# Performance work log

Measured on AMD Instinct MI355X. Metric: run time of the kernel, lower is better.

## Reference

```python
import jax, jax.numpy as jnp
import numpy as np
from jax import lax

D = 1024      # embedding_dim
E = 8         # num_experts
F = 4096      # expert_dim
TOP_K = 2


def setup_inputs() -> dict:
    key = jax.random.key(0)
    ks = jax.random.split(key, 8)
    s = 0.02
    return {
        "x": jax.random.normal(ks[0], (4, 2048, D), dtype=jnp.float32),
        "gate_w": jax.random.normal(ks[1], (D, E), dtype=jnp.float32) * s,
        "gate_b": jnp.zeros((E,), dtype=jnp.float32),
        "w1": jax.random.normal(ks[2], (E, D, F), dtype=jnp.float32) * s,
        "b1": jnp.zeros((E, F), dtype=jnp.float32),
        "w2": jax.random.normal(ks[3], (E, F, D), dtype=jnp.float32) * s,
        "b2": jnp.zeros((E, D), dtype=jnp.float32),
    }


def reference(x, gate_w, gate_b, w1, b1, w2, b2):
    B, S, _ = x.shape
    flat = x.reshape(-1, D)                      # [T, D]
    T = flat.shape[0]

    # Router: top-k gating with softmax over the selected logits (in fp32)
    logits = flat @ gate_w + gate_b              # [T, E]
    topv, topi = lax.top_k(logits, TOP_K)        # [T, K]
    topw = jax.nn.softmax(topv.astype(jnp.float32), axis=-1).astype(x.dtype)
    routing = jnp.zeros_like(logits).at[jnp.arange(T)[:, None], topi].set(topw)  # [T, E]

    # Per-expert MLP, combined with routing weights (zeros for unselected experts
    # reproduce the masked gather/scatter of the original exactly).
    def body(acc, params):
        W1e, b1e, W2e, b2e, we = params          # we: [T]
        h = jax.nn.gelu(flat @ W1e + b1e, approximate=False)  # [T, F]
        out = h @ W2e + b2e                      # [T, D]
        return acc + out * we[:, None], None

    init = jnp.zeros_like(flat)
    final, _ = lax.scan(body, init, (w1, b1, w2, b2, routing.T))
    return final.reshape(B, S, D)
```

## Files before the change

### kernel.cpp

```cpp
#include <hip/hip_runtime.h>
#include <hip/hip_bf16.h>
#include <math.h>


#define TK 8192
#define DDIM 1024
#define FDIM 4096
#define NEXP 8
#define MAXT128 136

typedef unsigned short u16;
typedef __attribute__((ext_vector_type(8))) short bf16x8;
typedef __attribute__((ext_vector_type(4))) float f32x4;

typedef const __attribute__((address_space(1))) unsigned int* gp_u32;
typedef __attribute__((address_space(3))) unsigned int* lp_u32;

__device__ __forceinline__ u16 f2bf(float f) {
  unsigned x = __float_as_uint(f);
  x += 0x7fffu + ((x >> 16) & 1u);
  return (u16)(x >> 16);
}

__device__ __forceinline__ float fast_gelu(float v) {
  float p = v * (1.5957691216f + 0.0713548162f * v * v);
  float t = __expf(p);
  return v * t * __builtin_amdgcn_rcpf(t + 1.0f);
}

__device__ __forceinline__ bf16x8 ldfrag(const char* base, int row, int slot) {
  return *(const bf16x8*)(base + row * 128 + ((slot ^ (row & 7)) << 4));
}

__global__ void router_kernel(const float* __restrict__ x, const float* __restrict__ gw,
                              const float* __restrict__ gb,
                              int* __restrict__ top_e, float* __restrict__ top_w) {
  const int t = blockIdx.x;
  const int l = threadIdx.x;
  const float* xr = x + (size_t)t * DDIM;
  float acc[8] = {0, 0, 0, 0, 0, 0, 0, 0};
  for (int k = l; k < DDIM; k += 64) {
    float xv = xr[k];
    const float4* g4 = (const float4*)(gw + (size_t)k * 8);
    float4 ga = g4[0], gbv = g4[1];
    acc[0] = fmaf(xv, ga.x, acc[0]);  acc[1] = fmaf(xv, ga.y, acc[1]);
    acc[2] = fmaf(xv, ga.z, acc[2]);  acc[3] = fmaf(xv, ga.w, acc[3]);
    acc[4] = fmaf(xv, gbv.x, acc[4]); acc[5] = fmaf(xv, gbv.y, acc[5]);
    acc[6] = fmaf(xv, gbv.z, acc[6]); acc[7] = fmaf(xv, gbv.w, acc[7]);
  }
#pragma unroll
  for (int e = 0; e < 8; ++e)
#pragma unroll
    for (int m = 32; m; m >>= 1) acc[e] += __shfl_xor(acc[e], m, 64);
  if (l == 0) {
    float lg[8];
#pragma unroll
    for (int e = 0; e < 8; ++e) lg[e] = acc[e] + gb[e];
    int i1 = 0;
#pragma unroll
    for (int e = 1; e < 8; ++e) if (lg[e] > lg[i1]) i1 = e;
    int i2 = (i1 == 0) ? 1 : 0;
#pragma unroll
    for (int e = 0; e < 8; ++e) if (e != i1 && lg[e] > lg[i2]) i2 = e;
    float e2 = __expf(lg[i2] - lg[i1]);
    float inv = 1.0f / (1.0f + e2);
    top_e[2 * t] = i1;      top_e[2 * t + 1] = i2;
    top_w[2 * t] = inv;     top_w[2 * t + 1] = e2 * inv;
  }
}

__global__ void count_kernel(const int* __restrict__ top_e, int* __restrict__ counts) {
  __shared__ int lc[8];
  if (threadIdx.x < 8) lc[threadIdx.x] = 0;
  __syncthreads();
  int t = blockIdx.x * 256 + threadIdx.x;
  if (t < TK) {
    atomicAdd(&lc[top_e[2 * t]], 1);
    atomicAdd(&lc[top_e[2 * t + 1]], 1);
  }
  __syncthreads();
  if (threadIdx.x < 8) atomicAdd(&counts[threadIdx.x], lc[threadIdx.x]);
}

__global__ void scan_kernel(const int* __restrict__ counts, int* __restrict__ seg,
                            int* __restrict__ cur, int* __restrict__ nt128,
                            int* __restrict__ map128) {
  if (threadIdx.x == 0) {
    int s = 0, i128 = 0;
    for (int e = 0; e < 8; ++e) {
      seg[e] = s; cur[e] = s;
      int c = counts[e];
      for (int mt = 0; mt * 128 < c; ++mt) map128[i128++] = (e << 16) | mt;
      s += c;
    }
    seg[8] = s;
    *nt128 = i128;
  }
}

__global__ void scatter_kernel(const int* __restrict__ top_e, const float* __restrict__ top_w,
                               int* __restrict__ cur, int* __restrict__ tok_ids,
                               float* __restrict__ tok_wt, int* __restrict__ inv) {
  __shared__ int lcnt[8];
  __shared__ int lbase[8];
  if (threadIdx.x < 8) lcnt[threadIdx.x] = 0;
  __syncthreads();
  int t = blockIdx.x * 256 + threadIdx.x;
  int e[2]; float wv[2]; int lpos[2];
  bool valid = t < TK;
  if (valid) {
#pragma unroll
    for (int j = 0; j < 2; ++j) {
      e[j] = top_e[2 * t + j];
      wv[j] = top_w[2 * t + j];
      lpos[j] = atomicAdd(&lcnt[e[j]], 1);
    }
  }
  __syncthreads();
  if (threadIdx.x < 8) lbase[threadIdx.x] = atomicAdd(&cur[threadIdx.x], lcnt[threadIdx.x]);
  __syncthreads();
  if (valid) {
#pragma unroll
    for (int j = 0; j < 2; ++j) {
      int slot = lbase[e[j]] + lpos[j];
      tok_ids[slot] = t;
      tok_wt[slot] = wv[j];
      inv[2 * t + j] = slot;
    }
  }
}

__global__ void gather_cast_kernel(const float* __restrict__ x, const int* __restrict__ tok_ids,
                                   uint4* __restrict__ Xg) {
  int idx = blockIdx.x * 256 + threadIdx.x;
  int row = idx >> 7, c8 = (idx & 127) * 8;
  long tok = tok_ids[row];
  const float4* p = (const float4*)(x + tok * DDIM + c8);
  float4 a = p[0], b = p[1];
  uint4 o;
  o.x = (unsigned)f2bf(a.x) | ((unsigned)f2bf(a.y) << 16);
  o.y = (unsigned)f2bf(a.z) | ((unsigned)f2bf(a.w) << 16);
  o.z = (unsigned)f2bf(b.x) | ((unsigned)f2bf(b.y) << 16);
  o.w = (unsigned)f2bf(b.z) | ((unsigned)f2bf(b.w) << 16);
  Xg[idx] = o;
}

__global__ void transpose_cast_kernel(const float* __restrict__ src, u16* __restrict__ dst,
                                      int K, int N) {
  __shared__ float tile[64][65];
  const int t = threadIdx.x;
  const float* s = src + (size_t)blockIdx.z * K * N + (size_t)(blockIdx.x * 64) * N + blockIdx.y * 64;
  u16* d = dst + (size_t)blockIdx.z * N * K + (size_t)(blockIdx.y * 64) * K + blockIdx.x * 64;
#pragma unroll
  for (int r = 0; r < 16; ++r) {
    int idx = r * 256 + t;
    int kk = idx >> 6, nn = idx & 63;
    tile[kk][nn] = s[(size_t)kk * N + nn];
  }
  __syncthreads();
#pragma unroll
  for (int r = 0; r < 16; ++r) {
    int idx = r * 256 + t;
    int nn = idx >> 6, kk = idx & 63;
    d[(size_t)nn * K + kk] = f2bf(tile[kk][nn]);
  }
}

template <int PHASE, int BM, int BN, int CHA, int CHB>
__global__ __launch_bounds__(256) void moe_gemm(
    const u16* __restrict__ A, const u16* __restrict__ Bt,
    const float* __restrict__ bias, u16* __restrict__ Hout, float* __restrict__ Out,
    u16* __restrict__ Yout,
    const int* __restrict__ seg_off, const int* __restrict__ counts,
    const int* __restrict__ ntiles, const int* __restrict__ tile_map,
    const int* __restrict__ tok_ids, const float* __restrict__ tok_wt,
    int K, int N) {
  constexpr int MF = BM / 32;
  constexpr int NF = BN / 32;

  const int NTm = *ntiles;
  const int nb = N / BN;
  const int nwg = NTm * nb;
  const int bid = (int)blockIdx.x;
  if (bid >= nwg) return;
  const int q = nwg >> 3, rr = nwg & 7;
  const int xcd = bid & 7, pos = bid >> 3;
  const int work = xcd * q + (xcd < rr ? xcd : rr) + pos;
  const int mtIdx = work / nb;
  const int n0 = (work % nb) * BN;

  const int ent = tile_map[mtIdx];
  const int e = ent >> 16;
  const int mt = ent & 0xffff;
  const int cnt = counts[e];
  const int seg = seg_off[e];

  const int t = threadIdx.x;
  const int w = t >> 6;
  const int l = t & 63;
  const int lr = l & 15, lh = l >> 4;
  const int wr = w >> 1, wc = w & 1;

  __shared__ u16 As[BM * 64];
  __shared__ u16 Bs[BN * 64];

  const u16* aga[CHA];
  const u16* bga[CHB];
  const u16* Bte = Bt + (size_t)e * N * K;
#pragma unroll
  for (int j = 0; j < CHA; ++j) {
    int c = t + 256 * j;
    int row = c >> 3;
    int js = (c & 7) ^ (row & 7);
    int m = mt * BM + row;
    if (m >= cnt) m = cnt - 1;
    aga[j] = A + (size_t)(seg + m) * K + js * 8;
  }
#pragma unroll
  for (int j = 0; j < CHB; ++j) {
    int c = t + 256 * j;
    int row = c >> 3;
    int js = (c & 7) ^ (row & 7);
    bga[j] = Bte + (size_t)(n0 + row) * K + js * 8;
  }

  f32x4 acc[MF][NF];
#pragma unroll
  for (int i = 0; i < MF; ++i)
#pragma unroll
    for (int j = 0; j < NF; ++j) acc[i][j] = (f32x4){0.f, 0.f, 0.f, 0.f};

  const int NT = K / 64;
  for (int kt = 0; kt < NT; ++kt) {
#pragma unroll
    for (int j = 0; j < CHA; ++j)
      __builtin_amdgcn_global_load_lds((gp_u32)(aga[j] + (size_t)kt * 64),
                                       (lp_u32)(&As[(t + 256 * j) * 8]), 16, 0, 0);
#pragma unroll
    for (int j = 0; j < CHB; ++j)
      __builtin_amdgcn_global_load_lds((gp_u32)(bga[j] + (size_t)kt * 64),
                                       (lp_u32)(&Bs[(t + 256 * j) * 8]), 16, 0, 0);
    __syncthreads();

    const char* AsB = (const char*)As;
    const char* BsB = (const char*)Bs;
#pragma unroll
    for (int kk = 0; kk < 2; ++kk) {
      const int slot = kk * 4 + lh;
      bf16x8 a[MF], b[NF];
#pragma unroll
      for (int mi = 0; mi < MF; ++mi)
        a[mi] = ldfrag(AsB, wr * (BM / 2) + mi * 16 + lr, slot);
#pragma unroll
      for (int ni = 0; ni < NF; ++ni)
        b[ni] = ldfrag(BsB, wc * (BN / 2) + ni * 16 + lr, slot);
#pragma unroll
      for (int mi = 0; mi < MF; ++mi)
#pragma unroll
        for (int ni = 0; ni < NF; ++ni)
          acc[mi][ni] = __builtin_amdgcn_mfma_f32_16x16x32_bf16(a[mi], b[ni], acc[mi][ni], 0, 0, 0);
    }
    __syncthreads();
  }

  const float* be = bias + (size_t)e * N;
#pragma unroll
  for (int mi = 0; mi < MF; ++mi)
#pragma unroll
    for (int r = 0; r < 4; ++r) {
      int m = mt * BM + wr * (BM / 2) + mi * 16 + lh * 4 + r;
      if (m < cnt) {
        if (PHASE == 1) {
          size_t hrow = (size_t)(seg + m) * N;
#pragma unroll
          for (int ni = 0; ni < NF; ++ni) {
            int col = n0 + wc * (BN / 2) + ni * 16 + lr;
            float v = acc[mi][ni][r] + be[col];
            Hout[hrow + col] = f2bf(fast_gelu(v));
          }
        } else {
          size_t yrow = (size_t)(seg + m) * N;
#pragma unroll
          for (int ni = 0; ni < NF; ++ni) {
            int col = n0 + wc * (BN / 2) + ni * 16 + lr;
            Yout[yrow + col] = f2bf(acc[mi][ni][r] + be[col]);
          }
        }
      }
    }
}

__global__ void combine_kernel(const u16* __restrict__ Y, const int* __restrict__ inv,
                               const float* __restrict__ top_w, float* __restrict__ out) {
  int idx = blockIdx.x * 256 + threadIdx.x;
  int t = idx >> 7, c = (idx & 127) * 8;
  int s0 = inv[2 * t], s1 = inv[2 * t + 1];
  float w0 = top_w[2 * t], w1 = top_w[2 * t + 1];
  const uint4 y0 = *(const uint4*)(Y + (size_t)s0 * DDIM + c);
  const uint4 y1 = *(const uint4*)(Y + (size_t)s1 * DDIM + c);
  float4 o0, o1;
#define LO(u) __uint_as_float((u) << 16)
#define HI(u) __uint_as_float((u) & 0xffff0000u)
  o0.x = w0 * LO(y0.x) + w1 * LO(y1.x); o0.y = w0 * HI(y0.x) + w1 * HI(y1.x);
  o0.z = w0 * LO(y0.y) + w1 * LO(y1.y); o0.w = w0 * HI(y0.y) + w1 * HI(y1.y);
  o1.x = w0 * LO(y0.z) + w1 * LO(y1.z); o1.y = w0 * HI(y0.z) + w1 * HI(y1.z);
  o1.z = w0 * LO(y0.w) + w1 * LO(y1.w); o1.w = w0 * HI(y0.w) + w1 * HI(y1.w);
#undef LO
#undef HI
  float4* op = (float4*)(out + (size_t)t * DDIM + c);
  op[0] = o0; op[1] = o1;
}

extern "C" void kernel_launch(void* const* d_in, const int* in_sizes, int n_in,
                              void* d_out, int out_size, void* d_ws, size_t ws_size,
                              hipStream_t stream) {
  const float* x  = (const float*)d_in[0];
  const float* gw = (const float*)d_in[1];
  const float* gb = (const float*)d_in[2];
  const float* w1 = (const float*)d_in[3];
  const float* b1 = (const float*)d_in[4];
  const float* w2 = (const float*)d_in[5];
  const float* b2 = (const float*)d_in[6];
  float* out = (float*)d_out;

  char* ws = (char*)d_ws;
  int*   counts  = (int*)(ws + 0);
  int*   cursors = (int*)(ws + 64);
  int*   seg     = (int*)(ws + 128);
  int*   nt128   = (int*)(ws + 192);
  int*   map128  = (int*)(ws + 1024);
  int*   top_e   = (int*)(ws + 4096);
  float* top_w   = (float*)(ws + 4096 + 65536);
  int*   tok_ids = (int*)(ws + 4096 + 131072);
  float* tok_wt  = (float*)(ws + 4096 + 196608);
  int*   invm    = (int*)(ws + 4096 + 262144);
  u16*   Xg      = (u16*)(ws + ((size_t)1 << 20));
  u16*   Y       = (u16*)(ws + ((size_t)1 << 20));
  u16*   H       = (u16*)(ws + ((size_t)36 << 20));
  u16*   wt      = (u16*)(ws + ((size_t)164 << 20));

  hipMemsetAsync(ws, 0, 256, stream);

  router_kernel<<<TK, 64, 0, stream>>>(x, gw, gb, top_e, top_w);
  count_kernel<<<TK / 256, 256, 0, stream>>>(top_e, counts);
  scan_kernel<<<1, 64, 0, stream>>>(counts, seg, cursors, nt128, map128);
  scatter_kernel<<<TK / 256, 256, 0, stream>>>(top_e, top_w, cursors, tok_ids, tok_wt, invm);
  gather_cast_kernel<<<2 * TK * 128 / 256, 256, 0, stream>>>(x, tok_ids, (uint4*)Xg);

  transpose_cast_kernel<<<dim3(DDIM / 64, FDIM / 64, NEXP), 256, 0, stream>>>(w1, wt, DDIM, FDIM);
  moe_gemm<1, 128, 128, 4, 4><<<dim3(MAXT128 * (FDIM / 128)), 256, 0, stream>>>(
      Xg, wt, b1, H, nullptr, nullptr, seg, counts, nt128, map128, tok_ids, tok_wt,
      DDIM, FDIM);
  transpose_cast_kernel<<<dim3(FDIM / 64, DDIM / 64, NEXP), 256, 0, stream>>>(w2, wt, FDIM, DDIM);

  moe_gemm<3, 128, 128, 4, 4><<<dim3(MAXT128 * (DDIM / 128)), 256, 0, stream>>>(
      H, wt, b2, nullptr, nullptr, Y, seg, counts, nt128, map128, tok_ids, tok_wt,
      FDIM, DDIM);
  combine_kernel<<<TK * 128 / 256, 256, 0, stream>>>(Y, invm, top_w, out);
}
```

Baseline: 516.2 us.

## Double-buffer LDS tiles in MoE GEMM and vectorize epilogue via swapped MFMA operands

```diff
diff --git a/kernel.cpp b/kernel.cpp
--- a/kernel.cpp
+++ b/kernel.cpp
@@ -169,11 +169,10 @@
 template <int PHASE, int BM, int BN, int CHA, int CHB>
 __global__ __launch_bounds__(256) void moe_gemm(
     const u16* __restrict__ A, const u16* __restrict__ Bt,
-    const float* __restrict__ bias, u16* __restrict__ Hout, float* __restrict__ Out,
+    const float* __restrict__ bias, u16* __restrict__ Hout,
     u16* __restrict__ Yout,
     const int* __restrict__ seg_off, const int* __restrict__ counts,
     const int* __restrict__ ntiles, const int* __restrict__ tile_map,
-    const int* __restrict__ tok_ids, const float* __restrict__ tok_wt,
     int K, int N) {
   constexpr int MF = BM / 32;
   constexpr int NF = BN / 32;
@@ -201,8 +200,8 @@
   const int lr = l & 15, lh = l >> 4;
   const int wr = w >> 1, wc = w & 1;
 
-  __shared__ u16 As[BM * 64];
-  __shared__ u16 Bs[BN * 64];
+  __shared__ u16 As[2][BM * 64];
+  __shared__ u16 Bs[2][BN * 64];
 
   const u16* aga[CHA];
   const u16* bga[CHB];
@@ -231,19 +230,29 @@
     for (int j = 0; j < NF; ++j) acc[i][j] = (f32x4){0.f, 0.f, 0.f, 0.f};
 
   const int NT = K / 64;
+
+#pragma unroll
+  for (int j = 0; j < CHA; ++j)
+    __builtin_amdgcn_global_load_lds((gp_u32)(aga[j]), (lp_u32)(&As[0][(t + 256 * j) * 8]), 16, 0, 0);
+#pragma unroll
+  for (int j = 0; j < CHB; ++j)
+    __builtin_amdgcn_global_load_lds((gp_u32)(bga[j]), (lp_u32)(&Bs[0][(t + 256 * j) * 8]), 16, 0, 0);
+  __syncthreads();
+
   for (int kt = 0; kt < NT; ++kt) {
-#pragma unroll
-    for (int j = 0; j < CHA; ++j)
-      __builtin_amdgcn_global_load_lds((gp_u32)(aga[j] + (size_t)kt * 64),
-                                       (lp_u32)(&As[(t + 256 * j) * 8]), 16, 0, 0);
-#pragma unroll
-    for (int j = 0; j < CHB; ++j)
-      __builtin_amdgcn_global_load_lds((gp_u32)(bga[j] + (size_t)kt * 64),
-                                       (lp_u32)(&Bs[(t + 256 * j) * 8]), 16, 0, 0);
-    __syncthreads();
-
-    const char* AsB = (const char*)As;
-    const char* BsB = (const char*)Bs;
+    const int cur = kt & 1;
+    if (kt + 1 < NT) {
+#pragma unroll
+      for (int j = 0; j < CHA; ++j)
+        __builtin_amdgcn_global_load_lds((gp_u32)(aga[j] + (size_t)(kt + 1) * 64),
+                                         (lp_u32)(&As[cur ^ 1][(t + 256 * j) * 8]), 16, 0, 0);
+#pragma unroll
+      for (int j = 0; j < CHB; ++j)
+        __builtin_amdgcn_global_load_lds((gp_u32)(bga[j] + (size_t)(kt + 1) * 64),
+                                         (lp_u32)(&Bs[cur ^ 1][(t + 256 * j) * 8]), 16, 0, 0);
+    }
+    const char* AsB = (const char*)&As[cur][0];
+    const char* BsB = (const char*)&Bs[cur][0];
 #pragma unroll
     for (int kk = 0; kk < 2; ++kk) {
       const int slot = kk * 4 + lh;
@@ -258,36 +267,37 @@
       for (int mi = 0; mi < MF; ++mi)
 #pragma unroll
         for (int ni = 0; ni < NF; ++ni)
-          acc[mi][ni] = __builtin_amdgcn_mfma_f32_16x16x32_bf16(a[mi], b[ni], acc[mi][ni], 0, 0, 0);
+          acc[mi][ni] = __builtin_amdgcn_mfma_f32_16x16x32_bf16(b[ni], a[mi], acc[mi][ni], 0, 0, 0);
     }
     __syncthreads();
   }
 
   const float* be = bias + (size_t)e * N;
 #pragma unroll
-  for (int mi = 0; mi < MF; ++mi)
-#pragma unroll
-    for (int r = 0; r < 4; ++r) {
-      int m = mt * BM + wr * (BM / 2) + mi * 16 + lh * 4 + r;
-      if (m < cnt) {
+  for (int mi = 0; mi < MF; ++mi) {
+    int m = mt * BM + wr * (BM / 2) + mi * 16 + lr;
+    if (m < cnt) {
+      size_t orow = (size_t)(seg + m) * N;
+#pragma unroll
+      for (int ni = 0; ni < NF; ++ni) {
+        int col = n0 + wc * (BN / 2) + ni * 16 + lh * 4;
+        float4 bv = *(const float4*)(be + col);
+        float v0 = acc[mi][ni][0] + bv.x;
+        float v1 = acc[mi][ni][1] + bv.y;
+        float v2 = acc[mi][ni][2] + bv.z;
+        float v3 = acc[mi][ni][3] + bv.w;
         if (PHASE == 1) {
-          size_t hrow = (size_t)(seg + m) * N;
-#pragma unroll
-          for (int ni = 0; ni < NF; ++ni) {
-            int col = n0 + wc * (BN / 2) + ni * 16 + lr;
-            float v = acc[mi][ni][r] + be[col];
-            Hout[hrow + col] = f2bf(fast_gelu(v));
-          }
-        } else {
-          size_t yrow = (size_t)(seg + m) * N;
-#pragma unroll
-          for (int ni = 0; ni < NF; ++ni) {
-            int col = n0 + wc * (BN / 2) + ni * 16 + lr;
-            Yout[yrow + col] = f2bf(acc[mi][ni][r] + be[col]);
-          }
+          v0 = fast_gelu(v0); v1 = fast_gelu(v1);
+          v2 = fast_gelu(v2); v3 = fast_gelu(v3);
         }
+        uint2 o;
+        o.x = (unsigned)f2bf(v0) | ((unsigned)f2bf(v1) << 16);
+        o.y = (unsigned)f2bf(v2) | ((unsigned)f2bf(v3) << 16);
+        u16* dst = (PHASE == 1) ? Hout : Yout;
+        *(uint2*)(dst + orow + col) = o;
       }
     }
+  }
 }
 
 __global__ void combine_kernel(const u16* __restrict__ Y, const int* __restrict__ inv,
@@ -349,12 +359,10 @@
 
   transpose_cast_kernel<<<dim3(DDIM / 64, FDIM / 64, NEXP), 256, 0, stream>>>(w1, wt, DDIM, FDIM);
   moe_gemm<1, 128, 128, 4, 4><<<dim3(MAXT128 * (FDIM / 128)), 256, 0, stream>>>(
-      Xg, wt, b1, H, nullptr, nullptr, seg, counts, nt128, map128, tok_ids, tok_wt,
-      DDIM, FDIM);
+      Xg, wt, b1, H, nullptr, seg, counts, nt128, map128, DDIM, FDIM);
   transpose_cast_kernel<<<dim3(FDIM / 64, DDIM / 64, NEXP), 256, 0, stream>>>(w2, wt, FDIM, DDIM);
 
   moe_gemm<3, 128, 128, 4, 4><<<dim3(MAXT128 * (DDIM / 128)), 256, 0, stream>>>(
-      H, wt, b2, nullptr, nullptr, Y, seg, counts, nt128, map128, tok_ids, tok_wt,
-      FDIM, DDIM);
+      H, wt, b2, nullptr, Y, seg, counts, nt128, map128, FDIM, DDIM);
   combine_kernel<<<TK * 128 / 256, 256, 0, stream>>>(Y, invm, top_w, out);
 }
```

After: 589.8 us. 1.14x slower.
